# Kernel tuning notes

Measured on AMD Instinct MI355X. Metric: run time of the kernel, lower is better.

The kernel has to match this reference:

```python
import jax, jax.numpy as jnp
import numpy as np

N_NODES = 100000
N_EDGES = 1000000
N_GRAPHS = 4096
F_IN = 9
H = 64


def setup_inputs() -> dict:
    key = jax.random.key(0)
    ks = jax.random.split(key, 12)
    x = jax.random.normal(ks[0], (N_NODES, F_IN), dtype=jnp.float32)
    edge_index = jax.random.randint(ks[1], (2, N_EDGES), 0, N_NODES, dtype=jnp.int64)
    batch = jnp.sort(jax.random.randint(ks[2], (N_NODES,), 0, N_GRAPHS, dtype=jnp.int64))
    def lin(k, fan_in, fan_out):
        s = 1.0 / np.sqrt(fan_in)
        return jax.random.uniform(k, (fan_in, fan_out), jnp.float32, -s, s)
    return {
        "x": x, "edge_index": edge_index, "batch": batch,
        "W1": lin(ks[3], F_IN, H), "b1": jnp.zeros((H,), jnp.float32),
        "W2": lin(ks[4], H, H),    "b2": jnp.zeros((H,), jnp.float32),
        "W3": lin(ks[5], H, H),    "b3": jnp.zeros((H,), jnp.float32),
        "W4": lin(ks[6], H, H),    "b4": jnp.zeros((H,), jnp.float32),
        "Wout": lin(ks[7], H, 1),  "bout": jnp.zeros((1,), jnp.float32),
    }


def reference(x, edge_index, batch, W1, b1, W2, b2, W3, b3, W4, b4, Wout, bout):
    N = x.shape[0]
    loops = jnp.arange(N, dtype=edge_index.dtype)
    src = jnp.concatenate([edge_index[0], loops])  # messages flow src -> dst (PyG source_to_target)
    dst = jnp.concatenate([edge_index[1], loops])
    # symmetric GCN normalization with self-loops: deg includes self-loop
    deg = jax.ops.segment_sum(jnp.ones_like(dst, dtype=x.dtype), dst, num_segments=N)
    dis = jax.lax.rsqrt(jnp.maximum(deg, 1.0))  # deg >= 1 thanks to self-loops
    norm = dis[src] * dis[dst]                  # [E+N]

    def gcn_conv(h, W, b):
        h = h @ W                                # transform first (PyG order)
        msgs = h[src] * norm[:, None]            # [E+N, H]
        return jax.ops.segment_sum(msgs, dst, num_segments=N) + b

    h = jax.nn.relu(gcn_conv(x, W1, b1))
    h = jax.nn.relu(gcn_conv(h, W2, b2))
    h = jax.nn.relu(gcn_conv(h, W3, b3))
    h = jax.nn.relu(gcn_conv(h, W4, b4))

    # global mean pool over graphs
    sums = jax.ops.segment_sum(h, batch, num_segments=N_GRAPHS)      # [G, H]
    counts = jax.ops.segment_sum(jnp.ones((N,), h.dtype), batch, num_segments=N_GRAPHS)
    pooled = sums / jnp.maximum(counts, 1.0)[:, None]
    return pooled @ Wout + bout                  # [G, 1]
```

## Files before the change

### kernel.cpp

```cpp
#include <hip/hip_runtime.h>
#include <hip/hip_fp16.h>


static inline size_t align256(size_t x){ return (x + 255) & ~size_t(255); }

#define CHUNK 2048

struct __align__(8)  h4v { __half2 a, b; };
struct __align__(16) h8v { __half2 a, b, c, d; };

typedef _Float16 f16x8 __attribute__((ext_vector_type(8)));
typedef float    f32x4 __attribute__((ext_vector_type(4)));

__global__ void k_zero(int* deg, float* gsum, int* gcount, int N, int G){
  int i = blockIdx.x*blockDim.x + threadIdx.x;
  if (i < N) deg[i] = 0;
  if (i < G){ gsum[i] = 0.f; gcount[i] = 0; }
}

__global__ void k_deg(const int* __restrict__ dst, const int* __restrict__ batch,
                      int* deg, int* gcount, int E, int N){
  int i = blockIdx.x*blockDim.x + threadIdx.x;
  if (i < E) atomicAdd(&deg[dst[i]], 1);
  if (i < N) atomicAdd(&gcount[batch[i]], 1);
}

__global__ void k_scanA(const int* __restrict__ deg, int* blockSums, int N){
  __shared__ int s[256];
  int t = threadIdx.x; int i = blockIdx.x*256 + t;
  s[t] = (i < N) ? deg[i] : 0;
  __syncthreads();
  for (int off=128; off>0; off>>=1){ if (t < off) s[t] += s[t+off]; __syncthreads(); }
  if (t==0) blockSums[blockIdx.x] = s[0];
}

__global__ void k_scanB(const int* __restrict__ blockSums, int* blockOffs, int NB){
  __shared__ int s[512];
  int t = threadIdx.x;
  int v = (t < NB) ? blockSums[t] : 0;
  s[t] = v; __syncthreads();
  for (int off=1; off<512; off<<=1){
    int add = (t>=off) ? s[t-off] : 0; __syncthreads();
    s[t] += add; __syncthreads();
  }
  if (t < NB) blockOffs[t] = s[t] - v;
}

__global__ void k_scanC(const int* __restrict__ deg, const int* __restrict__ blockOffs,
                        const float* __restrict__ x,
                        int* row_ptr, float* dis, float* __restrict__ xs, int N){
  __shared__ int s[256];
  int t = threadIdx.x; int i = blockIdx.x*256 + t;
  int v = (i < N) ? deg[i] : 0;
  s[t] = v; __syncthreads();
  for (int off=1; off<256; off<<=1){
    int add = (t>=off) ? s[t-off] : 0; __syncthreads();
    s[t] += add; __syncthreads();
  }
  if (i < N){
    int row = blockOffs[blockIdx.x] + s[t] - v;
    row_ptr[i] = row;
    float dv = rsqrtf((float)(v + 1));
    dis[i] = dv;
    #pragma unroll
    for (int k = 0; k < 9; k++) xs[i*9+k] = x[i*9+k]*dv;
    if (i == N-1) row_ptr[N] = blockOffs[blockIdx.x] + s[t];
  }
}

__global__ __launch_bounds__(256) void k_sortchunk(
    const int* __restrict__ src, const int* __restrict__ dst,
    int* __restrict__ binned, int* __restrict__ hoffC, int E){
  __shared__ int hcnt[1024];
  __shared__ int simg[CHUNK];
  int c = blockIdx.x, t = threadIdx.x;
  int e0 = c*CHUNK;
  int cnt = E - e0; if (cnt > CHUNK) cnt = CHUNK;

  for (int i = t; i < 1024; i += 256) hcnt[i] = 0;
  __syncthreads();

  int b_[8], r_[8], v_[8];
  #pragma unroll
  for (int j = 0; j < 8; j++){
    int i = t + j*256;
    if (i < cnt){
      int d = dst[e0+i];
      int s = src[e0+i];
      int b = d >> 7;
      b_[j] = b;
      r_[j] = atomicAdd(&hcnt[b], 1);
      v_[j] = (s << 7) | (d & 127);
    } else b_[j] = -1;
  }
  __syncthreads();

  int own[4];
  #pragma unroll
  for (int j = 0; j < 4; j++) own[j] = hcnt[t + j*256];
  for (int off = 1; off < 1024; off <<= 1){
    int nv[4];
    #pragma unroll
    for (int j = 0; j < 4; j++){
      int i = t + j*256;
      nv[j] = hcnt[i] + ((i >= off) ? hcnt[i-off] : 0);
    }
    __syncthreads();
    #pragma unroll
    for (int j = 0; j < 4; j++) hcnt[t + j*256] = nv[j];
    __syncthreads();
  }
  #pragma unroll
  for (int j = 0; j < 4; j++) hcnt[t + j*256] -= own[j];
  __syncthreads();

  for (int i = t; i < 783; i += 256) hoffC[c*783 + i] = hcnt[i];

  #pragma unroll
  for (int j = 0; j < 8; j++)
    if (b_[j] >= 0) simg[hcnt[b_[j]] + r_[j]] = v_[j];
  __syncthreads();

  for (int i = t; i < cnt; i += 256) binned[e0 + i] = simg[i];
}

__global__ __launch_bounds__(256) void k_gather(
    const int* __restrict__ binned, const int* __restrict__ hoffC,
    const int* __restrict__ row_ptr,
    int* __restrict__ csr, int N, int NC){
  __shared__ int lcur[128];
  int b = blockIdx.x, t = threadIdx.x;
  int n0 = b << 7;
  int nn = N - n0; if (nn > 128) nn = 128;
  if (t < nn) lcur[t] = row_ptr[n0 + t];
  __syncthreads();
  for (int c = t; c < NC; c += 256){
    int o0 = hoffC[c*783 + b];
    int o1 = hoffC[c*783 + b + 1];
    int base = c*CHUNK;
    for (int k = o0; k < o1; k++){
      int v = binned[base + k];
      int pos = atomicAdd(&lcur[v & 127], 1);
      csr[pos] = v >> 7;
    }
  }
}

__global__ void k_agg9(const float* __restrict__ xs, const float* __restrict__ dis,
                       const int* __restrict__ row_ptr, const int* __restrict__ csr,
                       float* __restrict__ xagg, int N){
  int tid = blockIdx.x*blockDim.x + threadIdx.x;
  if (tid >= N*9) return;
  int n = tid/9, f = tid - n*9;
  float dn = dis[n];
  int s0 = row_ptr[n], s1 = row_ptr[n+1];
  float a0 = xs[tid];
  float a1 = 0.f, a2 = 0.f, a3 = 0.f;
  int j = s0;
  for (; j + 3 < s1; j += 4){
    int e0 = csr[j], e1 = csr[j+1], e2 = csr[j+2], e3 = csr[j+3];
    a0 += xs[e0*9+f];
    a1 += xs[e1*9+f];
    a2 += xs[e2*9+f];
    a3 += xs[e3*9+f];
  }
  for (; j < s1; j++) a0 += xs[csr[j]*9+f];
  xagg[tid] = ((a0+a1)+(a2+a3))*dn;
}

__device__ __forceinline__ void mfma_epilogue(
    const _Float16* hlw, const f16x8 (&wf)[4][2],
    __half* __restrict__ mo, int wid, int nwaves, int N, int lane){
  int lm = lane & 15, lk = lane >> 4;
  f16x8 hb0 = *(const f16x8*)(hlw + lm*72 + lk*8);
  f16x8 hb1 = *(const f16x8*)(hlw + lm*72 + 32 + lk*8);
  int node = wid + lm*nwaves;
  bool ok = (node < N);
  __half* row = mo + (size_t)node*64;
  #pragma unroll
  for (int ft = 0; ft < 4; ft++){
    f32x4 acc = {0.f, 0.f, 0.f, 0.f};
    acc = __builtin_amdgcn_mfma_f32_16x16x32_f16(wf[ft][0], hb0, acc, 0, 0, 0);
    acc = __builtin_amdgcn_mfma_f32_16x16x32_f16(wf[ft][1], hb1, acc, 0, 0, 0);
    if (ok){
      h4v o;
      o.a = __floats2half2_rn(acc[0], acc[1]);
      o.b = __floats2half2_rn(acc[2], acc[3]);
      *(h4v*)(row + ft*16 + lk*4) = o;
    }
  }
}

#define LOAD_WFRAGS(Wn)                                                    \
  f16x8 wf[4][2];                                                          \
  { int lm_ = lane & 15, lk_ = lane >> 4;                                  \
    _Pragma("unroll") for (int ft = 0; ft < 4; ft++)                       \
    _Pragma("unroll") for (int kb = 0; kb < 2; kb++)                       \
    _Pragma("unroll") for (int j = 0; j < 8; j++)                          \
      wf[ft][kb][j] = (_Float16)Wn[(kb*32 + lk_*8 + j)*64 + ft*16 + lm_]; }

__global__ __launch_bounds__(256) void k_lin1_fused(
    const float* __restrict__ xagg, const float* __restrict__ W1,
    const float* __restrict__ b1, const float* __restrict__ dis,
    const float* __restrict__ W2, __half* __restrict__ mo, int N, int nwaves){
  __shared__ float W1l[576];
  __shared__ float b1l[64];
  __shared__ _Float16 hl[4][16*72];
  int t = threadIdx.x;
  for (int i = t; i < 576; i += 256) W1l[i] = W1[i];
  if (t < 64) b1l[t] = b1[t];
  __syncthreads();
  int lane = t & 63, w = t >> 6;
  int wid = (blockIdx.x*blockDim.x + t) >> 6;
  LOAD_WFRAGS(W2)
  _Float16* hlw = hl[w];
  for (int i = 0; i < 16; i++){
    int n = wid + i*nwaves;
    _Float16 hv = (_Float16)0.f;
    if (n < N){
      float acc = b1l[lane];
      #pragma unroll
      for (int k = 0; k < 9; k++) acc = fmaf(xagg[n*9+k], W1l[k*64+lane], acc);
      hv = (_Float16)(fmaxf(acc, 0.f) * dis[n]);
    }
    hlw[i*72 + lane] = hv;
  }
  mfma_epilogue(hlw, wf, mo, wid, nwaves, N, lane);
}

#define ACC8(g_)  do{ float2 t_;                                   \
  t_ = __half22float2((g_).a); acc0 += t_.x; acc1 += t_.y;         \
  t_ = __half22float2((g_).b); acc2 += t_.x; acc3 += t_.y;         \
  t_ = __half22float2((g_).c); acc4 += t_.x; acc5 += t_.y;         \
  t_ = __half22float2((g_).d); acc6 += t_.x; acc7 += t_.y; }while(0)

#define RED3(v)  do{ v += __shfl_xor(v, 8,64);                     \
                     v += __shfl_xor(v,16,64);                     \
                     v += __shfl_xor(v,32,64); }while(0)

#define AGG_ISSUE(n_, rp0_, rp1_, rn0_, rn1_, e0_, e1_, g0_, g1_, sf_, dn_) \
  do{                                                                      \
    int nn_ = (n_) + 2*nwaves;                                             \
    rn0_ = 0; rn1_ = 0;                                                    \
    if (nn_ < N){ rn0_ = row_ptr[nn_]; rn1_ = row_ptr[nn_+1]; }            \
    e0_ = -1; e1_ = -1;                                                    \
    if ((n_) < N){                                                         \
      sf_ = m[(size_t)(n_)*8 + q2];                                        \
      dn_ = dis[n_];                                                       \
      int j0_ = (rp0_) + sub, j1_ = (rp0_) + 8 + sub;                      \
      if (j0_ < (rp1_)) e0_ = csr[j0_];                                    \
      if (j1_ < (rp1_)) e1_ = csr[j1_];                                    \
      if (e0_ >= 0) g0_ = m[(size_t)e0_*8 + q2];                           \
      if (e1_ >= 0) g1_ = m[(size_t)e1_*8 + q2];                           \
    }                                                                      \
  }while(0)

#define AGG_ACCRED(n_, rp0_, rp1_, e0_, e1_, g0_, g1_, sf_, dn_)           \
      float acc0=0.f,acc1=0.f,acc2=0.f,acc3=0.f;                           \
      float acc4=0.f,acc5=0.f,acc6=0.f,acc7=0.f;                           \
      if (e0_ >= 0) ACC8(g0_);                                             \
      if (e1_ >= 0) ACC8(g1_);                                             \
      for (int j_ = (rp0_) + 16 + sub; j_ < (rp1_); j_ += 8){              \
        h8v gx_ = m[(size_t)csr[j_]*8 + q2]; ACC8(gx_);                    \
      }                                                                    \
      RED3(acc0); RED3(acc1); RED3(acc2); RED3(acc3);                      \
      RED3(acc4); RED3(acc5); RED3(acc6); RED3(acc7);                      \
      float2 s01=__half22float2((sf_).a), s23=__half22float2((sf_).b);     \
      float2 s45=__half22float2((sf_).c), s67=__half22float2((sf_).d);     \
      float r0 = fmaxf(fmaf(acc0 + s01.x, dn_, bb0.x), 0.f);               \
      float r1 = fmaxf(fmaf(acc1 + s01.y, dn_, bb0.y), 0.f);               \
      float r2 = fmaxf(fmaf(acc2 + s23.x, dn_, bb0.z), 0.f);               \
      float r3 = fmaxf(fmaf(acc3 + s23.y, dn_, bb0.w), 0.f);               \
      float r4 = fmaxf(fmaf(acc4 + s45.x, dn_, bb1.x), 0.f);               \
      float r5 = fmaxf(fmaf(acc5 + s45.y, dn_, bb1.y), 0.f);               \
      float r6 = fmaxf(fmaf(acc6 + s67.x, dn_, bb1.z), 0.f);               \
      float r7 = fmaxf(fmaf(acc7 + s67.y, dn_, bb1.w), 0.f);

#define AGG_REDUCE(n_, rp0_, rp1_, e0_, e1_, g0_, g1_, sf_, dn_, i_)       \
  do{                                                                      \
    if ((n_) < N){                                                         \
      AGG_ACCRED(n_, rp0_, rp1_, e0_, e1_, g0_, g1_, sf_, dn_)             \
      if (sub == 0){                                                       \
        h8v hv_;                                                           \
        hv_.a = __floats2half2_rn(r0*(dn_), r1*(dn_));                     \
        hv_.b = __floats2half2_rn(r2*(dn_), r3*(dn_));                     \
        hv_.c = __floats2half2_rn(r4*(dn_), r5*(dn_));                     \
        hv_.d = __floats2half2_rn(r6*(dn_), r7*(dn_));                     \
        *(h8v*)(hlw + (i_)*72 + q2*8) = hv_;                               \
      }                                                                    \
    } else if (sub == 0){                                                  \
      h8v z_; z_.a = __floats2half2_rn(0.f, 0.f);                          \
      z_.b = z_.a; z_.c = z_.a; z_.d = z_.a;                               \
      *(h8v*)(hlw + (i_)*72 + q2*8) = z_;                                  \
    }                                                                      \
  }while(0)

__global__ __launch_bounds__(256) void k_agg_fused(
    const h8v* __restrict__ m, const float* __restrict__ dis,
    const float* __restrict__ b, const float* __restrict__ Wn,
    const int* __restrict__ row_ptr, const int* __restrict__ csr,
    __half* __restrict__ mo, int N, int nwaves){
  __shared__ _Float16 hl[4][16*72];
  int t = threadIdx.x;
  int lane = t & 63, w = t >> 6;
  int sub = lane >> 3, q2 = lane & 7;
  int wid = (blockIdx.x*blockDim.x + t) >> 6;
  _Float16* hlw = hl[w];
  const float4* b4 = (const float4*)b;
  float4 bb0 = b4[q2*2], bb1 = b4[q2*2+1];

  int nA = wid,          rA0 = 0, rA1 = 0;
  int nB = wid + nwaves, rB0 = 0, rB1 = 0;
  if (nA < N){ rA0 = row_ptr[nA]; rA1 = row_ptr[nA+1]; }
  if (nB < N){ rB0 = row_ptr[nB]; rB1 = row_ptr[nB+1]; }
  int eA0, eA1, eB0, eB1, rnA0, rnA1, rnB0, rnB1;
  h8v gA0, gA1, sfA, gB0, gB1, sfB;
  float dnA = 0.f, dnB = 0.f;
  AGG_ISSUE(nA, rA0, rA1, rnA0, rnA1, eA0, eA1, gA0, gA1, sfA, dnA);
  for (int p = 0; p < 8; p++){
    AGG_ISSUE(nB, rB0, rB1, rnB0, rnB1, eB0, eB1, gB0, gB1, sfB, dnB);
    AGG_REDUCE(nA, rA0, rA1, eA0, eA1, gA0, gA1, sfA, dnA, 2*p);
    nA += 2*nwaves; rA0 = rnA0; rA1 = rnA1;
    if (p < 7)
      AGG_ISSUE(nA, rA0, rA1, rnA0, rnA1, eA0, eA1, gA0, gA1, sfA, dnA);
    AGG_REDUCE(nB, rB0, rB1, eB0, eB1, gB0, gB1, sfB, dnB, 2*p+1);
    nB += 2*nwaves; rB0 = rnB0; rB1 = rnB1;
  }
  LOAD_WFRAGS(Wn)
  mfma_epilogue(hlw, wf, mo, wid, nwaves, N, lane);
}

__global__ __launch_bounds__(256) void k_agg64_out(
    const h8v* __restrict__ m, const float* __restrict__ dis,
    const float* __restrict__ b, const float* __restrict__ Wout,
    const int* __restrict__ batch,
    const int* __restrict__ row_ptr, const int* __restrict__ csr,
    float* gsum, int N, int nwaves){
  int lane = threadIdx.x & 63;
  int sub = lane >> 3, q2 = lane & 7;
  int n = (blockIdx.x*blockDim.x + threadIdx.x) >> 6;
  if (n >= N) return;
  int rp0 = row_ptr[n], rp1 = row_ptr[n+1];
  const float4* b4 = (const float4*)b;
  const float4* wo4 = (const float4*)Wout;
  while (true){
    int nn = n + nwaves;
    int np0 = 0, np1 = 0;
    if (nn < N){ np0 = row_ptr[nn]; np1 = row_ptr[nn+1]; }
    h8v sf = m[(size_t)n*8 + q2];
    float dn = dis[n];
    int bg = batch[n];
    float acc0=0.f,acc1=0.f,acc2=0.f,acc3=0.f,acc4=0.f,acc5=0.f,acc6=0.f,acc7=0.f;
    int s1 = rp1;
    int j0 = rp0 + sub, j1 = rp0 + 8 + sub;
    if (j0 < s1){ h8v a = m[(size_t)csr[j0]*8 + q2]; ACC8(a); }
    if (j1 < s1){ h8v a = m[(size_t)csr[j1]*8 + q2]; ACC8(a); }
    for (int j = rp0 + 16 + sub; j < s1; j += 8){
      h8v a = m[(size_t)csr[j]*8 + q2]; ACC8(a);
    }
    RED3(acc0); RED3(acc1); RED3(acc2); RED3(acc3);
    RED3(acc4); RED3(acc5); RED3(acc6); RED3(acc7);
    float2 s01 = __half22float2(sf.a), s23 = __half22float2(sf.b);
    float2 s45 = __half22float2(sf.c), s67 = __half22float2(sf.d);
    float4 bb0 = b4[q2*2], bb1 = b4[q2*2+1];
    float4 w0 = wo4[q2*2], w1 = wo4[q2*2+1];
    float r0 = fmaxf(fmaf(acc0 + s01.x, dn, bb0.x), 0.f);
    float r1 = fmaxf(fmaf(acc1 + s01.y, dn, bb0.y), 0.f);
    float r2 = fmaxf(fmaf(acc2 + s23.x, dn, bb0.z), 0.f);
    float r3 = fmaxf(fmaf(acc3 + s23.y, dn, bb0.w), 0.f);
    float r4 = fmaxf(fmaf(acc4 + s45.x, dn, bb1.x), 0.f);
    float r5 = fmaxf(fmaf(acc5 + s45.y, dn, bb1.y), 0.f);
    float r6 = fmaxf(fmaf(acc6 + s67.x, dn, bb1.z), 0.f);
    float r7 = fmaxf(fmaf(acc7 + s67.y, dn, bb1.w), 0.f);
    float p = r0*w0.x + r1*w0.y + r2*w0.z + r3*w0.w
            + r4*w1.x + r5*w1.y + r6*w1.z + r7*w1.w;
    p += __shfl_xor(p,1,64); p += __shfl_xor(p,2,64); p += __shfl_xor(p,4,64);
    if (lane == 0) atomicAdd(&gsum[bg], p);
    if (nn >= N) break;
    n = nn; rp0 = np0; rp1 = np1;
  }
}

__global__ void k_final(const float* __restrict__ gsum, const int* __restrict__ gcount,
                        const float* __restrict__ bout, float* __restrict__ out, int G){
  int g = blockIdx.x*blockDim.x + threadIdx.x;
  if (g < G){
    int c = gcount[g];
    out[g] = gsum[g]/(float)(c > 0 ? c : 1) + bout[0];
  }
}

extern "C" void kernel_launch(void* const* d_in, const int* in_sizes, int n_in,
                              void* d_out, int out_size, void* d_ws, size_t ws_size,
                              hipStream_t stream){
  const float* x    = (const float*)d_in[0];
  const int*   ei   = (const int*)d_in[1];
  const int*   batch= (const int*)d_in[2];
  const float* W1 = (const float*)d_in[3];  const float* b1 = (const float*)d_in[4];
  const float* W2 = (const float*)d_in[5];  const float* b2 = (const float*)d_in[6];
  const float* W3 = (const float*)d_in[7];  const float* b3 = (const float*)d_in[8];
  const float* W4 = (const float*)d_in[9];  const float* b4 = (const float*)d_in[10];
  const float* Wout = (const float*)d_in[11]; const float* bout = (const float*)d_in[12];
  float* out = (float*)d_out;

  const int N = in_sizes[0]/9;
  const int E = in_sizes[1]/2;
  const int G = out_size;
  const int* src = ei;
  const int* dst = ei + E;

  char* ws = (char*)d_ws;
  size_t off = 0;
  auto alloc = [&](size_t bytes){ void* p = ws + off; off = align256(off + bytes); return p; };
  int*   deg      = (int*)  alloc((size_t)N*4);
  int*   row_ptr  = (int*)  alloc((size_t)(N+1)*4);
  int*   csr      = (int*)  alloc((size_t)E*4);
  float* dis      = (float*)alloc((size_t)N*4);
  const int NB  = (N + 255)/256;
  const int NBK = (N + 127)/128;
  const int NC  = (E + CHUNK-1)/CHUNK;
  int*   blockSums= (int*)  alloc((size_t)NB*4);
  int*   blockOffs= (int*)  alloc((size_t)NB*4);
  int*   hoffC    = (int*)  alloc((size_t)NC*783*4);
  float* gsum     = (float*)alloc((size_t)G*4);
  int*   gcount   = (int*)  alloc((size_t)G*4);
  __half* mA      = (__half*)alloc((size_t)N*64*2);
  __half* mB      = (__half*)alloc((size_t)N*64*2);
  int*   binned   = (int*)mA;
  float* xs       = (float*)mB;
  float* xagg     = xs + (size_t)N*9;

  const int EN = (E > N) ? E : N;
  const int AGG_BLOCKS = 2048;
  const int AGG_WAVES  = AGG_BLOCKS*4;

  k_zero     <<<(N+255)/256, 256, 0, stream>>>(deg, gsum, gcount, N, G);
  k_deg      <<<(EN+255)/256, 256, 0, stream>>>(dst, batch, deg, gcount, E, N);
  k_scanA    <<<NB, 256, 0, stream>>>(deg, blockSums, N);
  k_scanB    <<<1, 512, 0, stream>>>(blockSums, blockOffs, NB);
  k_scanC    <<<NB, 256, 0, stream>>>(deg, blockOffs, x, row_ptr, dis, xs, N);
  k_sortchunk<<<NC, 256, 0, stream>>>(src, dst, binned, hoffC, E);
  k_gather   <<<NBK, 256, 0, stream>>>(binned, hoffC, row_ptr, csr, N, NC);

  k_agg9  <<<(N*9+255)/256, 256, 0, stream>>>(xs, dis, row_ptr, csr, xagg, N);
  k_lin1_fused<<<AGG_BLOCKS, 256, 0, stream>>>(xagg, W1, b1, dis, W2, mA, N, AGG_WAVES);

  k_agg_fused<<<AGG_BLOCKS, 256, 0, stream>>>((const h8v*)mA, dis, b2, W3,
                                              row_ptr, csr, mB, N, AGG_WAVES);
  k_agg_fused<<<AGG_BLOCKS, 256, 0, stream>>>((const h8v*)mB, dis, b3, W4,
                                              row_ptr, csr, mA, N, AGG_WAVES);
  k_agg64_out<<<AGG_BLOCKS, 256, 0, stream>>>((const h8v*)mA, dis, b4, Wout, batch,
                                              row_ptr, csr, gsum, N, AGG_WAVES);

  k_final<<<(G+255)/256, 256, 0, stream>>>(gsum, gcount, bout, out, G);
}
```

Measured before the change: 341.4 us.

## Derive degrees and row pointers from chunk histograms, drop atomic degree pass

Removes the global atomic degree-count kernel and the three-stage node scan. Per-bucket totals now come from the existing sort-chunk histograms and are scanned in one block. Each gather block counts its 128 nodes' in-degrees in shared memory and writes row_ptr and dis itself. Graph counts come from a binary search over the sorted batch array in the final kernel instead of atomics. The cost is an extra pass over the binned edges in the gather kernel, a serial loop over all chunks per bucket, and a separate premultiply kernel.

```diff
diff --git a/kernel.cpp b/kernel.cpp
--- a/kernel.cpp
+++ b/kernel.cpp
@@ -12,60 +12,9 @@
 typedef _Float16 f16x8 __attribute__((ext_vector_type(8)));
 typedef float    f32x4 __attribute__((ext_vector_type(4)));
 
-__global__ void k_zero(int* deg, float* gsum, int* gcount, int N, int G){
+__global__ void k_zero(float* gsum, int G){
   int i = blockIdx.x*blockDim.x + threadIdx.x;
-  if (i < N) deg[i] = 0;
-  if (i < G){ gsum[i] = 0.f; gcount[i] = 0; }
-}
-
-__global__ void k_deg(const int* __restrict__ dst, const int* __restrict__ batch,
-                      int* deg, int* gcount, int E, int N){
-  int i = blockIdx.x*blockDim.x + threadIdx.x;
-  if (i < E) atomicAdd(&deg[dst[i]], 1);
-  if (i < N) atomicAdd(&gcount[batch[i]], 1);
-}
-
-__global__ void k_scanA(const int* __restrict__ deg, int* blockSums, int N){
-  __shared__ int s[256];
-  int t = threadIdx.x; int i = blockIdx.x*256 + t;
-  s[t] = (i < N) ? deg[i] : 0;
-  __syncthreads();
-  for (int off=128; off>0; off>>=1){ if (t < off) s[t] += s[t+off]; __syncthreads(); }
-  if (t==0) blockSums[blockIdx.x] = s[0];
-}
-
-__global__ void k_scanB(const int* __restrict__ blockSums, int* blockOffs, int NB){
-  __shared__ int s[512];
-  int t = threadIdx.x;
-  int v = (t < NB) ? blockSums[t] : 0;
-  s[t] = v; __syncthreads();
-  for (int off=1; off<512; off<<=1){
-    int add = (t>=off) ? s[t-off] : 0; __syncthreads();
-    s[t] += add; __syncthreads();
-  }
-  if (t < NB) blockOffs[t] = s[t] - v;
-}
-
-__global__ void k_scanC(const int* __restrict__ deg, const int* __restrict__ blockOffs,
-                        const float* __restrict__ x,
-                        int* row_ptr, float* dis, float* __restrict__ xs, int N){
-  __shared__ int s[256];
-  int t = threadIdx.x; int i = blockIdx.x*256 + t;
-  int v = (i < N) ? deg[i] : 0;
-  s[t] = v; __syncthreads();
-  for (int off=1; off<256; off<<=1){
-    int add = (t>=off) ? s[t-off] : 0; __syncthreads();
-    s[t] += add; __syncthreads();
-  }
-  if (i < N){
-    int row = blockOffs[blockIdx.x] + s[t] - v;
-    row_ptr[i] = row;
-    float dv = rsqrtf((float)(v + 1));
-    dis[i] = dv;
-    #pragma unroll
-    for (int k = 0; k < 9; k++) xs[i*9+k] = x[i*9+k]*dv;
-    if (i == N-1) row_ptr[N] = blockOffs[blockIdx.x] + s[t];
-  }
+  if (i < G) gsum[i] = 0.f;
 }
 
 __global__ __launch_bounds__(256) void k_sortchunk(
@@ -124,15 +73,70 @@
   for (int i = t; i < cnt; i += 256) binned[e0 + i] = simg[i];
 }
 
-__global__ __launch_bounds__(256) void k_gather(
+__global__ void k_bktsum(const int* __restrict__ hoffC, int* __restrict__ btot,
+                         int NC, int NBK){
+  int b = blockIdx.x*blockDim.x + threadIdx.x;
+  if (b >= NBK) return;
+  int tot = 0;
+  for (int c = 0; c < NC; c++){
+    int h0 = hoffC[c*783 + b];
+    int h1 = hoffC[c*783 + b + 1];
+    tot += h1 - h0;
+  }
+  btot[b] = tot;
+}
+
+__global__ __launch_bounds__(1024) void k_bktscan(
+    const int* __restrict__ btot, int* __restrict__ bbase,
+    int* __restrict__ row_ptr, int NBK, int N, int E){
+  __shared__ int s[1024];
+  int t = threadIdx.x;
+  int v = (t < NBK) ? btot[t] : 0;
+  s[t] = v; __syncthreads();
+  for (int off = 1; off < 1024; off <<= 1){
+    int add = (t >= off) ? s[t-off] : 0; __syncthreads();
+    s[t] += add; __syncthreads();
+  }
+  if (t < NBK) bbase[t] = s[t] - v;
+  if (t == 0) row_ptr[N] = E;
+}
+
+__global__ __launch_bounds__(256) void k_gather2(
     const int* __restrict__ binned, const int* __restrict__ hoffC,
-    const int* __restrict__ row_ptr,
+    const int* __restrict__ bbase,
+    int* __restrict__ row_ptr, float* __restrict__ dis,
     int* __restrict__ csr, int N, int NC){
   __shared__ int lcur[128];
+  __shared__ int lscan[128];
   int b = blockIdx.x, t = threadIdx.x;
   int n0 = b << 7;
   int nn = N - n0; if (nn > 128) nn = 128;
-  if (t < nn) lcur[t] = row_ptr[n0 + t];
+  if (t < 128) lcur[t] = 0;
+  __syncthreads();
+  for (int c = t; c < NC; c += 256){
+    int o0 = hoffC[c*783 + b];
+    int o1 = hoffC[c*783 + b + 1];
+    int base = c*CHUNK;
+    for (int k = o0; k < o1; k++)
+      atomicAdd(&lcur[binned[base + k] & 127], 1);
+  }
+  __syncthreads();
+  int degv = (t < 128) ? lcur[t] : 0;
+  if (t < 128) lscan[t] = degv;
+  __syncthreads();
+  for (int off = 1; off < 128; off <<= 1){
+    int add = (t < 128 && t >= off) ? lscan[t-off] : 0;
+    __syncthreads();
+    if (t < 128) lscan[t] += add;
+    __syncthreads();
+  }
+  int bb = bbase[b];
+  if (t < nn){
+    int row = bb + lscan[t] - degv;
+    row_ptr[n0 + t] = row;
+    dis[n0 + t] = rsqrtf((float)(degv + 1));
+    lcur[t] = row;
+  }
   __syncthreads();
   for (int c = t; c < NC; c += 256){
     int o0 = hoffC[c*783 + b];
@@ -144,6 +148,12 @@
       csr[pos] = v >> 7;
     }
   }
+}
+
+__global__ void k_premul(const float* __restrict__ x, const float* __restrict__ dis,
+                         float* __restrict__ xs, int N){
+  int i = blockIdx.x*blockDim.x + threadIdx.x;
+  if (i < N*9) xs[i] = x[i]*dis[i/9];
 }
 
 __global__ void k_agg9(const float* __restrict__ xs, const float* __restrict__ dis,
@@ -381,13 +391,18 @@
   }
 }
 
-__global__ void k_final(const float* __restrict__ gsum, const int* __restrict__ gcount,
-                        const float* __restrict__ bout, float* __restrict__ out, int G){
+__global__ void k_final(const float* __restrict__ gsum, const int* __restrict__ batch,
+                        const float* __restrict__ bout, float* __restrict__ out,
+                        int G, int N){
   int g = blockIdx.x*blockDim.x + threadIdx.x;
-  if (g < G){
-    int c = gcount[g];
-    out[g] = gsum[g]/(float)(c > 0 ? c : 1) + bout[0];
-  }
+  if (g >= G) return;
+  int lo = 0, hi = N;
+  while (lo < hi){ int mid = (lo+hi)>>1; if (batch[mid] <  g) lo = mid+1; else hi = mid; }
+  int lb = lo;
+  lo = 0; hi = N;
+  while (lo < hi){ int mid = (lo+hi)>>1; if (batch[mid] <= g) lo = mid+1; else hi = mid; }
+  int c = lo - lb;
+  out[g] = gsum[g]/(float)(c > 0 ? c : 1) + bout[0];
 }
 
 extern "C" void kernel_launch(void* const* d_in, const int* in_sizes, int n_in,
@@ -412,36 +427,31 @@
   char* ws = (char*)d_ws;
   size_t off = 0;
   auto alloc = [&](size_t bytes){ void* p = ws + off; off = align256(off + bytes); return p; };
-  int*   deg      = (int*)  alloc((size_t)N*4);
   int*   row_ptr  = (int*)  alloc((size_t)(N+1)*4);
   int*   csr      = (int*)  alloc((size_t)E*4);
   float* dis      = (float*)alloc((size_t)N*4);
-  const int NB  = (N + 255)/256;
   const int NBK = (N + 127)/128;
   const int NC  = (E + CHUNK-1)/CHUNK;
-  int*   blockSums= (int*)  alloc((size_t)NB*4);
-  int*   blockOffs= (int*)  alloc((size_t)NB*4);
   int*   hoffC    = (int*)  alloc((size_t)NC*783*4);
+  int*   btot     = (int*)  alloc((size_t)NBK*4);
+  int*   bbase    = (int*)  alloc((size_t)NBK*4);
   float* gsum     = (float*)alloc((size_t)G*4);
-  int*   gcount   = (int*)  alloc((size_t)G*4);
   __half* mA      = (__half*)alloc((size_t)N*64*2);
   __half* mB      = (__half*)alloc((size_t)N*64*2);
   int*   binned   = (int*)mA;
   float* xs       = (float*)mB;
   float* xagg     = xs + (size_t)N*9;
 
-  const int EN = (E > N) ? E : N;
   const int AGG_BLOCKS = 2048;
   const int AGG_WAVES  = AGG_BLOCKS*4;
 
-  k_zero     <<<(N+255)/256, 256, 0, stream>>>(deg, gsum, gcount, N, G);
-  k_deg      <<<(EN+255)/256, 256, 0, stream>>>(dst, batch, deg, gcount, E, N);
-  k_scanA    <<<NB, 256, 0, stream>>>(deg, blockSums, N);
-  k_scanB    <<<1, 512, 0, stream>>>(blockSums, blockOffs, NB);
-  k_scanC    <<<NB, 256, 0, stream>>>(deg, blockOffs, x, row_ptr, dis, xs, N);
+  k_zero     <<<(G+255)/256, 256, 0, stream>>>(gsum, G);
   k_sortchunk<<<NC, 256, 0, stream>>>(src, dst, binned, hoffC, E);
-  k_gather   <<<NBK, 256, 0, stream>>>(binned, hoffC, row_ptr, csr, N, NC);
-
+  k_bktsum   <<<(NBK+255)/256, 256, 0, stream>>>(hoffC, btot, NC, NBK);
+  k_bktscan  <<<1, 1024, 0, stream>>>(btot, bbase, row_ptr, NBK, N, E);
+  k_gather2  <<<NBK, 256, 0, stream>>>(binned, hoffC, bbase, row_ptr, dis, csr, N, NC);
+
+  k_premul<<<(N*9+255)/256, 256, 0, stream>>>(x, dis, xs, N);
   k_agg9  <<<(N*9+255)/256, 256, 0, stream>>>(xs, dis, row_ptr, csr, xagg, N);
   k_lin1_fused<<<AGG_BLOCKS, 256, 0, stream>>>(xagg, W1, b1, dis, W2, mA, N, AGG_WAVES);
 
@@ -452,5 +462,5 @@
   k_agg64_out<<<AGG_BLOCKS, 256, 0, stream>>>((const h8v*)mA, dis, b4, Wout, batch,
                                               row_ptr, csr, gsum, N, AGG_WAVES);
 
-  k_final<<<(G+255)/256, 256, 0, stream>>>(gsum, gcount, bout, out, G);
-}
+  k_final<<<(G+255)/256, 256, 0, stream>>>(gsum, batch, bout, out, G, N);
+}
```

New measurement: 379.8 us. +11.3%, slower.
